# Performance work log

Measured on AMD Instinct MI355X. Metric: run time of the kernel, lower is better.

The kernel has to match this reference:

```python
import jax, jax.numpy as jnp
import numpy as np

# --- module hyperparams (match init_kwargs) ---
IN_F, OUT_F, K, GROUP, STRIDE, PAD = 64, 64, 3, 8, 1, 1
NUM_KERNELS = int(np.ceil(OUT_F / GROUP))          # 8 groups
IN_DPC = int(np.ceil(IN_F / NUM_KERNELS))          # in-ch per group = 8
WORKING = GROUP * NUM_KERNELS                      # 64 conv out channels
WORKING_IN = IN_DPC * NUM_KERNELS                  # 64 conv in channels
B, H, W = 16, 192, 192


def setup_inputs() -> dict:
    key = jax.random.key(0)
    k1, k2, k3, k4, k5, k6 = jax.random.split(key, 6)
    x = jax.random.normal(k1, (B, IN_F, H, W), jnp.float32)
    # grouped conv weight, torch layout (out, in/groups, kh, kw), no bias
    conv_w = jax.random.normal(k2, (WORKING, WORKING_IN // NUM_KERNELS, K, K), jnp.float32) * 0.05
    A = jax.random.uniform(k3, (1, WORKING, 1, 1), jnp.float32)
    D = jax.random.uniform(k4, (1, WORKING, 1, 1), jnp.float32)
    bias = jax.random.uniform(k5, (1, WORKING, 1, 1), jnp.float32)
    perm = jax.random.permutation(k6, WORKING).astype(jnp.int32)  # torch.randperm buffer
    return {"x": x, "conv_w": conv_w, "A": A, "D": D, "bias": bias, "perm": perm}


def reference(x, conv_w, A, D, bias, perm):
    # channel pad to working_in (no-op for these dims, kept for fidelity)
    z = jnp.pad(x, ((0, 0), (0, WORKING_IN - IN_F), (0, 0), (0, 0)))
    # grouped conv2d, no bias
    z = jax.lax.conv_general_dilated(
        z, conv_w,
        window_strides=(STRIDE, STRIDE),
        padding=((PAD, PAD), (PAD, PAD)),
        dimension_numbers=("NCHW", "OIHW", "NCHW"),
        feature_group_count=NUM_KERNELS,
    )
    z = z * A                      # elementwise scale
    z = jnp.fft.fft(z, axis=1)     # FFT along channel dim -> complex64
    z = z * D                      # diagonal (real) scale in frequency space
    z = jnp.fft.ifft(z, axis=1)    # back to 'channel' space (still complex)
    z = z + bias
    # channel permutation gather, slice to out_f, normalize
    z = jnp.take(z, perm, axis=1)[:, :OUT_F]
    return z / jnp.sqrt(jnp.float32(OUT_F))
```

## Files before the change

kernel.cpp:

```cpp
#include <hip/hip_runtime.h>
#include <math.h>

#define Bn 16
#define Cn 64
#define Hn 192
#define Wn 192
#define NPIX (Bn * Cn * Hn * Wn)
#define NBLKS 512
#define WCOLS 98
#define SLOTB (WCOLS * 128)

typedef short bf16x8 __attribute__((ext_vector_type(8)));
typedef float f32x16 __attribute__((ext_vector_type(16)));
typedef __attribute__((address_space(1))) const unsigned int as1_u32;
typedef __attribute__((address_space(3))) unsigned int as3_u32;

__device__ __align__(16) unsigned short g_Ms[9 * 64 * 64];
__device__ __align__(16) float g_b2[64];

static __device__ __forceinline__ unsigned short f2bf(float f) {
    union { float f; unsigned u; } x; x.f = f;
    unsigned r = x.u + 0x7fffu + ((x.u >> 16) & 1u);
    return (unsigned short)(r >> 16);
}

__global__ void acdc_precompute(const float* __restrict__ cw, const float* __restrict__ A,
                                const float* __restrict__ D, const float* __restrict__ bias,
                                const int* __restrict__ perm) {
    __shared__ float mre[64];
    int p = blockIdx.x;
    int t = threadIdx.x;
    if (t < 64) {
        float re = 0.f;
        for (int k = 0; k < 64; ++k) {
            int a = (k * t) & 63;
            re += D[k] * cosf((float)a * 0.0981747704246810387f);
        }
        mre[t] = re;
    }
    __syncthreads();
    int pp = perm[p];
    for (int k0 = t; k0 < 576; k0 += 256) {
        int sp = k0 >> 6, c = k0 & 63;
        int g = c >> 3, cil = c & 7;
        float val = 0.f;
        for (int o = 0; o < 8; ++o) {
            int oc = g * 8 + o;
            float gco = mre[(pp - oc + 64) & 63] * A[oc] * (0.125f / 64.0f);
            val += gco * cw[(oc * 8 + cil) * 9 + sp];
        }
        g_Ms[((sp * 64 + p) << 6) + (((g ^ (p & 7)) << 3) | cil)] = f2bf(val);
    }
    if (p == 0 && t < 64)
        g_b2[t] = bias[perm[t]] * 0.125f;
}

__global__ __launch_bounds__(512, 2)
void acdc_main(const float* __restrict__ x, float* __restrict__ out) {
    __shared__ __align__(16) unsigned short Mlds[9 * 64 * 64];
    __shared__ __align__(16) unsigned char xsb[4 * SLOTB];

    int tid = threadIdx.x;
    int lane = tid & 63, wv = tid >> 6;
    int Lb = (blockIdx.x & 7) * (NBLKS / 8) + (blockIdx.x >> 3);
    int bb = Lb >> 5;
    int band = (Lb >> 1) & 15;
    int half = Lb & 1;
    int h0 = band * 12;
    int cbase = half * 96;

    #pragma unroll
    for (int k = 0; k < 9; ++k) {
        int chunk = wv + k * 8;
        if (chunk < 72) {
            const unsigned char* src = (const unsigned char*)g_Ms + chunk * 1024 + lane * 16;
            __builtin_amdgcn_global_load_lds((as1_u32*)(const void*)src,
                (as3_u32*)(void*)((unsigned char*)Mlds + chunk * 1024), 16, 0, 0);
        }
    }

    const float* xb = x + (size_t)bb * Cn * Hn * Wn;

    for (int k = 0; k < 7; ++k) {
        int idx = tid + (k << 9);
        if (idx >= 3328) break;
        int cp_lo = idx & 3;
        int f = (idx >> 2) % 26;
        int r4 = idx / 104;
        int rr = r4 & 3, cp_hi = r4 >> 2;
        int cp = cp_hi * 4 + cp_lo;
        int gi = h0 - 1 + rr;
        int gc0 = cbase + 4 * f - 4;
        float av[4] = {0.f,0.f,0.f,0.f}, bv[4] = {0.f,0.f,0.f,0.f};
        bool giok = (unsigned)gi < (unsigned)Hn;
        const float* r0 = xb + ((size_t)(2 * cp) * Hn + (giok ? gi : 0)) * Wn;
        const float* r1 = r0 + Hn * Wn;
        if (giok) {
            if (gc0 >= 0 && gc0 <= Wn - 4) {
                float4 a = *(const float4*)(r0 + gc0);
                float4 b = *(const float4*)(r1 + gc0);
                av[0]=a.x; av[1]=a.y; av[2]=a.z; av[3]=a.w;
                bv[0]=b.x; bv[1]=b.y; bv[2]=b.z; bv[3]=b.w;
            } else {
                #pragma unroll
                for (int j = 0; j < 4; ++j) {
                    int gc = gc0 + j;
                    if ((unsigned)gc < (unsigned)Wn) { av[j] = r0[gc]; bv[j] = r1[gc]; }
                }
            }
        }
        int slot = rr;
        int chunk = cp >> 2, sub = (cp & 3) * 4;
        #pragma unroll
        for (int j = 0; j < 4; ++j) {
            int c2 = 4 * f + j - 3;
            if ((unsigned)c2 >= (unsigned)WCOLS) continue;
            unsigned u;
            asm("v_cvt_pk_bf16_f32 %0, %1, %2" : "=v"(u) : "v"(av[j]), "v"(bv[j]));
            int key = (c2 + (c2 >> 3) + 3 * slot) & 7;
            *(unsigned*)(xsb + slot * SLOTB + c2 * 128 + ((chunk ^ key) << 4) + sub) = u;
        }
    }
    __syncthreads();

    int l31 = lane & 31, lh = lane >> 5;

    float4 va[4], vb[4];
    for (int t = 0; t < 6; ++t) {
        int hb = h0 + 2 * t;

        if (t < 5) {
            #pragma unroll
            for (int k = 0; k < 4; ++k) {
                int idx = tid + (k << 9);
                va[k] = (float4){0.f,0.f,0.f,0.f};
                vb[k] = (float4){0.f,0.f,0.f,0.f};
                if (idx >= 1664) continue;
                int cp_lo = idx & 3;
                int f = (idx >> 2) % 26;
                int r2 = idx / 104;
                int rr = r2 & 1, cp_hi = r2 >> 1;
                int cp = cp_hi * 4 + cp_lo;
                int gi = hb + 3 + rr;
                int gc0 = cbase + 4 * f - 4;
                bool giok = (unsigned)gi < (unsigned)Hn;
                const float* r0 = xb + ((size_t)(2 * cp) * Hn + (giok ? gi : 0)) * Wn;
                const float* r1 = r0 + Hn * Wn;
                if (giok) {
                    if (gc0 >= 0 && gc0 <= Wn - 4) {
                        va[k] = *(const float4*)(r0 + gc0);
                        vb[k] = *(const float4*)(r1 + gc0);
                    } else {
                        float t0[4] = {0,0,0,0}, t1[4] = {0,0,0,0};
                        #pragma unroll
                        for (int j = 0; j < 4; ++j) {
                            int gc = gc0 + j;
                            if ((unsigned)gc < (unsigned)Wn) { t0[j] = r0[gc]; t1[j] = r1[gc]; }
                        }
                        va[k] = (float4){t0[0], t0[1], t0[2], t0[3]};
                        vb[k] = (float4){t1[0], t1[1], t1[2], t1[3]};
                    }
                }
            }
        }

        if (wv < 6) {
            int rr = wv & 1;
            int nt = wv >> 1;
            f32x16 acc0, acc1;
            #pragma unroll
            for (int e = 0; e < 16; ++e) { acc0[e] = 0.f; acc1[e] = 0.f; }

            #pragma unroll
            for (int sp = 0; sp < 9; ++sp) {
                const int dy = sp / 3, dx = sp % 3;
                int v = (2 * t + rr + dy) & 3;
                int c2 = nt * 32 + l31 + dx;
                int key = (c2 + (c2 >> 3) + 3 * v) & 7;
                const unsigned char* bbase = xsb + v * SLOTB + c2 * 128;
                const unsigned char* abase = (const unsigned char*)Mlds + sp * 8192 + l31 * 128;
                #pragma unroll
                for (int ks = 0; ks < 4; ++ks) {
                    int o = 2 * ks + lh;
                    bf16x8 bfr = *(const bf16x8*)(bbase + ((o ^ key) << 4));
                    const unsigned char* ap = abase + ((o ^ (l31 & 7)) << 4);
                    bf16x8 am0 = *(const bf16x8*)ap;
                    bf16x8 am1 = *(const bf16x8*)(ap + 4096);
                    __builtin_amdgcn_s_setprio(1);
                    acc0 = __builtin_amdgcn_mfma_f32_32x32x16_bf16(am0, bfr, acc0, 0, 0, 0);
                    acc1 = __builtin_amdgcn_mfma_f32_32x32x16_bf16(am1, bfr, acc1, 0, 0, 0);
                    __builtin_amdgcn_s_setprio(0);
                }
            }

            int h = hb + rr;
            int pxg = cbase + nt * 32 + l31;
            #pragma unroll
            for (int r = 0; r < 16; ++r) {
                int chq = (r & 3) + 8 * (r >> 2) + 4 * lh;
                out[(((size_t)(bb * Cn + chq)) * Hn + h) * Wn + pxg]      = acc0[r] + g_b2[chq];
                out[(((size_t)(bb * Cn + 32 + chq)) * Hn + h) * Wn + pxg] = acc1[r] + g_b2[32 + chq];
            }
        }

        __syncthreads();

        if (t < 5) {
            #pragma unroll
            for (int k = 0; k < 4; ++k) {
                int idx = tid + (k << 9);
                if (idx >= 1664) continue;
                int cp_lo = idx & 3;
                int f = (idx >> 2) % 26;
                int r2 = idx / 104;
                int rr = r2 & 1, cp_hi = r2 >> 1;
                int cp = cp_hi * 4 + cp_lo;
                int vslot = (2 * t + rr) & 3;
                int chunk = cp >> 2, sub = (cp & 3) * 4;
                float v0[4] = {va[k].x, va[k].y, va[k].z, va[k].w};
                float v1[4] = {vb[k].x, vb[k].y, vb[k].z, vb[k].w};
                #pragma unroll
                for (int j = 0; j < 4; ++j) {
                    int c2 = 4 * f + j - 3;
                    if ((unsigned)c2 >= (unsigned)WCOLS) continue;
                    unsigned u;
                    asm("v_cvt_pk_bf16_f32 %0, %1, %2" : "=v"(u) : "v"(v0[j]), "v"(v1[j]));
                    int key = (c2 + (c2 >> 3) + 3 * vslot) & 7;
                    *(unsigned*)(xsb + vslot * SLOTB + c2 * 128 + ((chunk ^ key) << 4) + sub) = u;
                }
            }
        }
        __syncthreads();
    }
}

extern "C" void kernel_launch(void* const* d_in, const int* in_sizes, int n_in,
                              void* d_out, int out_size, void* d_ws, size_t ws_size,
                              hipStream_t stream) {
    const float* x    = (const float*)d_in[0];
    const float* cw   = (const float*)d_in[1];
    const float* A    = (const float*)d_in[2];
    const float* D    = (const float*)d_in[3];
    const float* bias = (const float*)d_in[4];
    const int*   perm = (const int*)d_in[5];

    acdc_precompute<<<dim3(64), dim3(256), 0, stream>>>(cw, A, D, bias, perm);
    acdc_main<<<dim3(NBLKS), dim3(512), 0, stream>>>(x, (float*)d_out);
}
```

Baseline: 100.7 us.

## Warp-specialize main kernel with dedicated loader waves and 6-slot row ring

Blocks grow to 1024 threads. Waves 0-5 run the MFMA convolution while the remaining waves fetch the next two input rows from global memory and write them as bf16 into a ring buffer that grows from 4 to 6 slots. This replaces the old scheme, where every wave prefetched into registers and then stored to LDS behind an extra barrier, so there is now one barrier per row pair. The aim is to overlap global loads with compute; the cost is more LDS (close to the per-CU limit) and a tighter per-thread register budget at 1024 threads.

```diff
diff --git a/kernel.cpp b/kernel.cpp
--- a/kernel.cpp
+++ b/kernel.cpp
@@ -55,10 +55,10 @@
         g_b2[t] = bias[perm[t]] * 0.125f;
 }
 
-__global__ __launch_bounds__(512, 2)
+__global__ __launch_bounds__(1024)
 void acdc_main(const float* __restrict__ x, float* __restrict__ out) {
     __shared__ __align__(16) unsigned short Mlds[9 * 64 * 64];
-    __shared__ __align__(16) unsigned char xsb[4 * SLOTB];
+    __shared__ __align__(16) unsigned char xsb[6 * SLOTB];
 
     int tid = threadIdx.x;
     int lane = tid & 63, wv = tid >> 6;
@@ -70,8 +70,8 @@
     int cbase = half * 96;
 
     #pragma unroll
-    for (int k = 0; k < 9; ++k) {
-        int chunk = wv + k * 8;
+    for (int k = 0; k < 5; ++k) {
+        int chunk = wv + k * 16;
         if (chunk < 72) {
             const unsigned char* src = (const unsigned char*)g_Ms + chunk * 1024 + lane * 16;
             __builtin_amdgcn_global_load_lds((as1_u32*)(const void*)src,
@@ -81,8 +81,8 @@
 
     const float* xb = x + (size_t)bb * Cn * Hn * Wn;
 
-    for (int k = 0; k < 7; ++k) {
-        int idx = tid + (k << 9);
+    for (int k = 0; k < 4; ++k) {
+        int idx = tid + (k << 10);
         if (idx >= 3328) break;
         int cp_lo = idx & 3;
         int f = (idx >> 2) % 26;
@@ -125,44 +125,8 @@
 
     int l31 = lane & 31, lh = lane >> 5;
 
-    float4 va[4], vb[4];
     for (int t = 0; t < 6; ++t) {
         int hb = h0 + 2 * t;
-
-        if (t < 5) {
-            #pragma unroll
-            for (int k = 0; k < 4; ++k) {
-                int idx = tid + (k << 9);
-                va[k] = (float4){0.f,0.f,0.f,0.f};
-                vb[k] = (float4){0.f,0.f,0.f,0.f};
-                if (idx >= 1664) continue;
-                int cp_lo = idx & 3;
-                int f = (idx >> 2) % 26;
-                int r2 = idx / 104;
-                int rr = r2 & 1, cp_hi = r2 >> 1;
-                int cp = cp_hi * 4 + cp_lo;
-                int gi = hb + 3 + rr;
-                int gc0 = cbase + 4 * f - 4;
-                bool giok = (unsigned)gi < (unsigned)Hn;
-                const float* r0 = xb + ((size_t)(2 * cp) * Hn + (giok ? gi : 0)) * Wn;
-                const float* r1 = r0 + Hn * Wn;
-                if (giok) {
-                    if (gc0 >= 0 && gc0 <= Wn - 4) {
-                        va[k] = *(const float4*)(r0 + gc0);
-                        vb[k] = *(const float4*)(r1 + gc0);
-                    } else {
-                        float t0[4] = {0,0,0,0}, t1[4] = {0,0,0,0};
-                        #pragma unroll
-                        for (int j = 0; j < 4; ++j) {
-                            int gc = gc0 + j;
-                            if ((unsigned)gc < (unsigned)Wn) { t0[j] = r0[gc]; t1[j] = r1[gc]; }
-                        }
-                        va[k] = (float4){t0[0], t0[1], t0[2], t0[3]};
-                        vb[k] = (float4){t1[0], t1[1], t1[2], t1[3]};
-                    }
-                }
-            }
-        }
 
         if (wv < 6) {
             int rr = wv & 1;
@@ -174,7 +138,7 @@
             #pragma unroll
             for (int sp = 0; sp < 9; ++sp) {
                 const int dy = sp / 3, dx = sp % 3;
-                int v = (2 * t + rr + dy) & 3;
+                int v = 2 * t + rr + dy; if (v >= 6) v -= 6; if (v >= 6) v -= 6;
                 int c2 = nt * 32 + l31 + dx;
                 int key = (c2 + (c2 >> 3) + 3 * v) & 7;
                 const unsigned char* bbase = xsb + v * SLOTB + c2 * 128;
@@ -201,35 +165,49 @@
                 out[(((size_t)(bb * Cn + chq)) * Hn + h) * Wn + pxg]      = acc0[r] + g_b2[chq];
                 out[(((size_t)(bb * Cn + 32 + chq)) * Hn + h) * Wn + pxg] = acc1[r] + g_b2[32 + chq];
             }
-        }
-
-        __syncthreads();
-
-        if (t < 5) {
-            #pragma unroll
-            for (int k = 0; k < 4; ++k) {
-                int idx = tid + (k << 9);
-                if (idx >= 1664) continue;
-                int cp_lo = idx & 3;
-                int f = (idx >> 2) % 26;
-                int r2 = idx / 104;
-                int rr = r2 & 1, cp_hi = r2 >> 1;
+        } else if (t < 5) {
+            for (int k = 0; k < 3; ++k) {
+                int sidx = (tid - 384) + k * 640;
+                if (sidx >= 1664) break;
+                int cp_lo = sidx & 3;
+                int f = (sidx >> 2) % 26;
+                int r2 = sidx / 104;
+                int rr2 = r2 & 1, cp_hi = r2 >> 1;
                 int cp = cp_hi * 4 + cp_lo;
-                int vslot = (2 * t + rr) & 3;
+                int gi = hb + 3 + rr2;
+                int gc0 = cbase + 4 * f - 4;
+                float av[4] = {0.f,0.f,0.f,0.f}, bv[4] = {0.f,0.f,0.f,0.f};
+                bool giok = (unsigned)gi < (unsigned)Hn;
+                const float* r0 = xb + ((size_t)(2 * cp) * Hn + (giok ? gi : 0)) * Wn;
+                const float* r1 = r0 + Hn * Wn;
+                if (giok) {
+                    if (gc0 >= 0 && gc0 <= Wn - 4) {
+                        float4 a = *(const float4*)(r0 + gc0);
+                        float4 b = *(const float4*)(r1 + gc0);
+                        av[0]=a.x; av[1]=a.y; av[2]=a.z; av[3]=a.w;
+                        bv[0]=b.x; bv[1]=b.y; bv[2]=b.z; bv[3]=b.w;
+                    } else {
+                        #pragma unroll
+                        for (int j = 0; j < 4; ++j) {
+                            int gc = gc0 + j;
+                            if ((unsigned)gc < (unsigned)Wn) { av[j] = r0[gc]; bv[j] = r1[gc]; }
+                        }
+                    }
+                }
+                int vslot = 2 * t + 4 + rr2; while (vslot >= 6) vslot -= 6;
                 int chunk = cp >> 2, sub = (cp & 3) * 4;
-                float v0[4] = {va[k].x, va[k].y, va[k].z, va[k].w};
-                float v1[4] = {vb[k].x, vb[k].y, vb[k].z, vb[k].w};
                 #pragma unroll
                 for (int j = 0; j < 4; ++j) {
                     int c2 = 4 * f + j - 3;
                     if ((unsigned)c2 >= (unsigned)WCOLS) continue;
                     unsigned u;
-                    asm("v_cvt_pk_bf16_f32 %0, %1, %2" : "=v"(u) : "v"(v0[j]), "v"(v1[j]));
+                    asm("v_cvt_pk_bf16_f32 %0, %1, %2" : "=v"(u) : "v"(av[j]), "v"(bv[j]));
                     int key = (c2 + (c2 >> 3) + 3 * vslot) & 7;
                     *(unsigned*)(xsb + vslot * SLOTB + c2 * 128 + ((chunk ^ key) << 4) + sub) = u;
                 }
             }
         }
+
         __syncthreads();
     }
 }
@@ -245,5 +223,5 @@
     const int*   perm = (const int*)d_in[5];
 
     acdc_precompute<<<dim3(64), dim3(256), 0, stream>>>(cw, A, D, bias, perm);
-    acdc_main<<<dim3(NBLKS), dim3(512), 0, stream>>>(x, (float*)d_out);
-}
+    acdc_main<<<dim3(NBLKS), dim3(1024), 0, stream>>>(x, (float*)d_out);
+}
```

After: 103.1 us. 2.4% more time.
